# Kernel optimization log

Hardware: AMD Instinct MI355X
Metric: run time of the kernel (lower is better)

## Reference

```python
import jax, jax.numpy as jnp
import numpy as np

T, H, I, E, TOPK = 8192, 2048, 4096, 8, 2

def setup_inputs() -> dict:
    key = jax.random.key(0)
    k1, k2, k3, k4 = jax.random.split(key, 4)
    x = jax.random.normal(k1, (T, H), dtype=jnp.float32)
    gate_w = jax.random.normal(k2, (E, H), dtype=jnp.float32) * 0.02
    ws = jax.random.normal(k3, (E, 2 * I, H), dtype=jnp.float32) * 0.02
    w2s = jax.random.normal(k4, (E, H, I), dtype=jnp.float32) * 0.02
    return {"x": x, "gate_w": gate_w, "ws": ws, "w2s": w2s, "top_k": TOPK}

def reference(x, gate_w, ws, w2s, top_k):
    num_tokens = x.shape[0]
    num_experts = ws.shape[0]
    inter = w2s.shape[2]
    # --- router (fused_topk): softmax -> top-k -> renormalize ---
    logits = x @ gate_w.T                       # [T, E]
    probs = jax.nn.softmax(logits, axis=-1)
    topk_w, topk_ids = jax.lax.top_k(probs, top_k)   # [T, K]
    if top_k > 1:
        topk_w = topk_w / jnp.sum(topk_w, axis=-1, keepdims=True)
    # dense combine-weights [E, T]: sum of routing weights per (token, expert)
    tok = jnp.arange(num_tokens)
    cw = jnp.zeros((num_tokens, num_experts), dtype=x.dtype)
    cw = cw.at[tok[:, None], topk_ids].add(topk_w)
    cw = cw.T                                   # [E, T]
    # --- fused_experts: per-expert gated-SiLU MLP, weighted combine ---
    def body(acc, inp):
        e_ws, e_w2, e_cw = inp                  # [2I,H], [H,I], [T]
        gu = x @ e_ws.T                         # [T, 2I]
        g, u = gu[:, :inter], gu[:, inter:]
        h = jax.nn.silu(g) * u                  # SiluAndMul
        out = h @ e_w2.T                        # [T, H]
        return acc + e_cw[:, None] * out, None
    init = jnp.zeros_like(x)
    final, _ = jax.lax.scan(body, init, (ws, w2s, cw))
    return final
```

## Files before the change

### kernel.cpp

```cpp
#include <hip/hip_runtime.h>
#include <hip/hip_fp16.h>
#include <cstdint>
#include <cstddef>

#define TTOK 8192
#define HD   2048
#define ID   4096
#define NE   8
#define NPAIR (TTOK * 2)
#define PADROWS 18432
#define RBMAX 72

typedef _Float16 h8 __attribute__((ext_vector_type(8)));
typedef float    f4 __attribute__((ext_vector_type(4)));

#define VMWAIT(n) asm volatile("s_waitcnt vmcnt(" #n ")" ::: "memory")
#define MEMFENCE  asm volatile("" ::: "memory")
#define BAR()     __builtin_amdgcn_s_barrier()

__device__ __forceinline__ void async_cp16(const void* g, void* l) {
  __builtin_amdgcn_global_load_lds(
      (const __attribute__((address_space(1))) unsigned int*)g,
      (__attribute__((address_space(3))) unsigned int*)l, 16, 0, 0);
}

__device__ __forceinline__ f4 zero4() { f4 z = {0.f, 0.f, 0.f, 0.f}; return z; }

template <bool NT>
__global__ void cvt_kernel(const float* __restrict__ src, _Float16* __restrict__ dst, size_t n) {
  size_t stride = (size_t)gridDim.x * blockDim.x * 8;
  for (size_t i = ((size_t)blockIdx.x * blockDim.x + threadIdx.x) * 8; i < n; i += stride) {
    const float4* s = (const float4*)(src + i);
    float4 a = s[0], b = s[1];
    h8 o;
    o[0] = (_Float16)a.x; o[1] = (_Float16)a.y; o[2] = (_Float16)a.z; o[3] = (_Float16)a.w;
    o[4] = (_Float16)b.x; o[5] = (_Float16)b.y; o[6] = (_Float16)b.z; o[7] = (_Float16)b.w;
    if constexpr (NT) __builtin_nontemporal_store(o, (h8*)(dst + i));
    else *(h8*)(dst + i) = o;
  }
}

__global__ __launch_bounds__(256) void gate_kernel(
    const float* __restrict__ x, const float* __restrict__ gw,
    int* __restrict__ counts, int* __restrict__ tids, float* __restrict__ tw) {
  int lane = threadIdx.x & 63;
  int t = blockIdx.x * 4 + (threadIdx.x >> 6);
  const float* xr = x + (size_t)t * HD;
  float acc[NE];
#pragma unroll
  for (int e = 0; e < NE; e++) acc[e] = 0.f;
  for (int j = lane; j < HD; j += 64) {
    float xv = xr[j];
#pragma unroll
    for (int e = 0; e < NE; e++) acc[e] += xv * gw[e * HD + j];
  }
#pragma unroll
  for (int off = 32; off > 0; off >>= 1) {
#pragma unroll
    for (int e = 0; e < NE; e++) acc[e] += __shfl_xor(acc[e], off, 64);
  }
  if (lane == 0) {
    int e0 = 0; float v0 = acc[0];
#pragma unroll
    for (int e = 1; e < NE; e++) if (acc[e] > v0) { v0 = acc[e]; e0 = e; }
    int e1 = -1; float v1 = -1e30f;
#pragma unroll
    for (int e = 0; e < NE; e++) if (e != e0 && acc[e] > v1) { v1 = acc[e]; e1 = e; }
    float b = __expf(v1 - v0);
    float w0 = 1.f / (1.f + b);
    tids[2 * t] = e0; tids[2 * t + 1] = e1;
    tw[2 * t] = w0;   tw[2 * t + 1] = b * w0;
    atomicAdd(&counts[e0], 1); atomicAdd(&counts[e1], 1);
  }
}

__global__ void scan_kernel(const int* __restrict__ counts, int* __restrict__ offs,
                            int* __restrict__ cursor) {
  if (threadIdx.x == 0 && blockIdx.x == 0) {
    int off = 0;
    for (int e = 0; e < NE; e++) {
      offs[e] = off; cursor[e] = off;
      off += ((counts[e] + 255) >> 8) << 8;
    }
    offs[NE] = off;
  }
}

__global__ void scatter_kernel(const int* __restrict__ tids, const float* __restrict__ tw,
                               int* __restrict__ cursor, int* __restrict__ perm,
                               float* __restrict__ pw, int* __restrict__ pairpos) {
  int t = blockIdx.x * 256 + threadIdx.x;
#pragma unroll
  for (int k = 0; k < 2; k++) {
    int e = tids[2 * t + k];
    int pos = atomicAdd(&cursor[e], 1);
    perm[pos] = t; pw[pos] = tw[2 * t + k];
    pairpos[2 * t + k] = pos;
  }
}

__global__ void padfill_kernel(const int* __restrict__ counts, const int* __restrict__ offs,
                               int* __restrict__ perm) {
  int s = blockIdx.x * 256 + threadIdx.x;
#pragma unroll
  for (int e = 0; e < NE; e++) {
    if (s >= offs[e] + counts[e] && s < offs[e + 1]) perm[s] = -1;
  }
}

#define LA(BB, H) ((BB) * 65536 + (H) * 16384)
#define LB(BB, H) ((BB) * 65536 + 32768 + (H) * 16384)
#define RD(boff) (*(const h8*)(smem + (boff)))

#define LOAD_AF(BB, MH) do { \
  af[0][0] = RD(LA(BB,MH) + amoff + 0*2048 + sa0); \
  af[0][1] = RD(LA(BB,MH) + amoff + 0*2048 + sa1); \
  af[1][0] = RD(LA(BB,MH) + amoff + 1*2048 + sa0); \
  af[1][1] = RD(LA(BB,MH) + amoff + 1*2048 + sa1); \
  af[2][0] = RD(LA(BB,MH) + amoff + 2*2048 + sa0); \
  af[2][1] = RD(LA(BB,MH) + amoff + 2*2048 + sa1); \
  af[3][0] = RD(LA(BB,MH) + amoff + 3*2048 + sa0); \
  af[3][1] = RD(LA(BB,MH) + amoff + 3*2048 + sa1); } while (0)

#define LOAD_BF(BB, NH) do { \
  bf[0][0] = RD(LB(BB,NH) + bnoff + 0*2048 + sa0); \
  bf[0][1] = RD(LB(BB,NH) + bnoff + 0*2048 + sa1); \
  bf[1][0] = RD(LB(BB,NH) + bnoff + 1*2048 + sa0); \
  bf[1][1] = RD(LB(BB,NH) + bnoff + 1*2048 + sa1); } while (0)

#define MM(MH,NH,M,N) \
  acc[MH][NH][M][N] = __builtin_amdgcn_mfma_f32_16x16x32_f16(af[M][0], bf[N][0], acc[MH][NH][M][N], 0, 0, 0); \
  acc[MH][NH][M][N] = __builtin_amdgcn_mfma_f32_16x16x32_f16(af[M][1], bf[N][1], acc[MH][NH][M][N], 0, 0, 0);

#define MFMAQ(MH,NH) do { __builtin_amdgcn_s_setprio(1); \
  MM(MH,NH,0,0) MM(MH,NH,0,1) MM(MH,NH,1,0) MM(MH,NH,1,1) \
  MM(MH,NH,2,0) MM(MH,NH,2,1) MM(MH,NH,3,0) MM(MH,NH,3,1) \
  __builtin_amdgcn_s_setprio(0); } while (0)

#define STG(gp, ldsbyte, kt) do { \
  async_cp16(gp[0] + (size_t)(kt) * 64, smem + (ldsbyte) + (wid * 2 + 0) * 1024 + lane * 16); \
  async_cp16(gp[1] + (size_t)(kt) * 64, smem + (ldsbyte) + (wid * 2 + 1) * 1024 + lane * 16); } while (0)

#define ACC_ZERO() do { \
  _Pragma("unroll") for (int mh = 0; mh < 2; mh++) \
  _Pragma("unroll") for (int nh = 0; nh < 2; nh++) \
  _Pragma("unroll") for (int m = 0; m < 4; m++) \
  _Pragma("unroll") for (int n = 0; n < 2; n++) acc[mh][nh][m][n] = zero4(); } while (0)

#define KLOOP(NI) \
  STG(gA[0], LA(0,0), 0); STG(gA[1], LA(0,1), 0); \
  STG(gB[0], LB(0,0), 0); STG(gB[1], LB(0,1), 0); \
  STG(gA[0], LA(1,0), 1); STG(gB[1], LB(1,1), 1); \
  VMWAIT(4); \
  BAR(); \
  for (int i = 0; i < (NI); ++i) { \
    bool last = (i == (NI) - 1); \
    int kt1 = 2 * i + 1, kt2 = 2 * i + 2, kt3 = 2 * i + 3; \
     \
    MEMFENCE; LOAD_AF(0,0); LOAD_BF(0,0); \
    STG(gA[1], LA(1,1), kt1); STG(gB[0], LB(1,0), kt1); \
    BAR(); MEMFENCE; MFMAQ(0,0); BAR(); \
     \
    MEMFENCE; LOAD_BF(0,1); \
    BAR(); MEMFENCE; MFMAQ(0,1); BAR(); \
     \
    MEMFENCE; LOAD_AF(0,1); \
    if (!last) STG(gA[0], LA(0,0), kt2); \
    BAR(); MEMFENCE; MFMAQ(1,1); BAR(); \
     \
    MEMFENCE; LOAD_BF(0,0); \
    if (!last) { STG(gB[1], LB(0,1), kt2); VMWAIT(4); } else { VMWAIT(0); } \
    BAR(); MEMFENCE; MFMAQ(1,0); BAR(); \
     \
    MEMFENCE; LOAD_AF(1,0); LOAD_BF(1,0); \
    if (!last) { STG(gA[1], LA(0,1), kt2); STG(gB[0], LB(0,0), kt2); } \
    BAR(); MEMFENCE; MFMAQ(0,0); BAR(); \
     \
    MEMFENCE; LOAD_BF(1,1); \
    BAR(); MEMFENCE; MFMAQ(0,1); BAR(); \
     \
    MEMFENCE; LOAD_AF(1,1); \
    if (!last) STG(gA[0], LA(1,0), kt3); \
    BAR(); MEMFENCE; MFMAQ(1,1); BAR(); \
     \
    MEMFENCE; LOAD_BF(1,0); \
    if (!last) { STG(gB[1], LB(1,1), kt3); VMWAIT(4); } \
    BAR(); MEMFENCE; MFMAQ(1,0); BAR(); \
  }

__device__ __forceinline__ int expert_of(const int* offs, int row0) {
  int e = 0;
#pragma unroll
  for (int k = 1; k < NE; k++) if (offs[k] <= row0) e = k;
  return e;
}

__global__ __launch_bounds__(512, 2) void gemm1_kernel(
    const _Float16* __restrict__ xh, const _Float16* __restrict__ wsh,
    const int* __restrict__ offs, const int* __restrict__ perm,
    _Float16* __restrict__ hb) {
  int lin = blockIdx.x + gridDim.x * blockIdx.y;
  int oct = lin >> 8, x8 = lin & 7, bx = (lin >> 3) & 31;
  int gyy = oct * 8 + x8;
  int row0 = gyy << 8;
  if (row0 >= offs[NE]) return;
  int e = expert_of(offs, row0);
  int n0 = bx << 7;

  __shared__ char smem[131072];
  int tid = threadIdx.x, lane = tid & 63, wid = tid >> 6;
  int wm = wid >> 2, wn = wid & 3;
  int lr = lane & 15, ks = lane >> 4;
  int sa0 = lr * 128 + (((ks)     ^ (lr & 7)) << 4);
  int sa1 = lr * 128 + (((ks + 4) ^ (lr & 7)) << 4);
  int amoff = wm * 8192;
  int bnoff = wn * 4096;

  int srow = wid * 16 + (lane >> 3);
  int scol = ((lane & 7) ^ (lane >> 3)) * 8;
  const _Float16* gA[2][2]; const _Float16* gB[2][2];
#pragma unroll
  for (int h = 0; h < 2; h++)
#pragma unroll
    for (int j = 0; j < 2; j++) {
      int r = row0 + h * 128 + srow + j * 8;
      int pv = perm[r]; if (pv < 0) pv = 0;
      gA[h][j] = xh + (size_t)pv * HD + scol;
      gB[h][j] = wsh + ((size_t)e * 2 * ID + (size_t)h * ID + n0 + srow + j * 8) * HD + scol;
    }

  f4 acc[2][2][4][2];
  h8 af[4][2], bf[2][2];
  ACC_ZERO();

  KLOOP(16)

#pragma unroll
  for (int mh = 0; mh < 2; mh++)
#pragma unroll
    for (int m = 0; m < 4; m++)
#pragma unroll
      for (int n = 0; n < 2; n++)
#pragma unroll
        for (int r = 0; r < 4; r++) {
          float g = acc[mh][0][m][n][r], u = acc[mh][1][m][n][r];
          float hv = g / (1.f + __expf(-g)) * u;
          int row = row0 + mh * 128 + wm * 64 + m * 16 + ks * 4 + r;
          int col = n0 + wn * 32 + n * 16 + lr;
          __builtin_nontemporal_store((_Float16)hv, hb + (size_t)row * ID + col);
        }
}

__global__ __launch_bounds__(512, 2) void gemm2_kernel(
    const _Float16* __restrict__ hb, const _Float16* __restrict__ w2h,
    const int* __restrict__ offs, _Float16* __restrict__ hb2) {
  int lin = blockIdx.x + gridDim.x * blockIdx.y;
  int oct = lin >> 6, x8 = lin & 7, bx = (lin >> 3) & 7;
  int gyy = oct * 8 + x8;
  int row0 = gyy << 8;
  if (row0 >= offs[NE]) return;
  int e = expert_of(offs, row0);
  int n0 = bx << 8;
  int kh = blockIdx.z;
  size_t k0 = (size_t)kh * 2048;

  __shared__ char smem[131072];
  int tid = threadIdx.x, lane = tid & 63, wid = tid >> 6;
  int wm = wid >> 2, wn = wid & 3;
  int lr = lane & 15, ks = lane >> 4;
  int sa0 = lr * 128 + (((ks)     ^ (lr & 7)) << 4);
  int sa1 = lr * 128 + (((ks + 4) ^ (lr & 7)) << 4);
  int amoff = wm * 8192;
  int bnoff = wn * 4096;

  int srow = wid * 16 + (lane >> 3);
  int scol = ((lane & 7) ^ (lane >> 3)) * 8;
  const _Float16* gA[2][2]; const _Float16* gB[2][2];
#pragma unroll
  for (int h = 0; h < 2; h++)
#pragma unroll
    for (int j = 0; j < 2; j++) {
      gA[h][j] = hb + ((size_t)(row0 + h * 128 + srow + j * 8)) * ID + k0 + scol;
      gB[h][j] = w2h + ((size_t)e * HD + n0 + h * 128 + srow + j * 8) * ID + k0 + scol;
    }

  f4 acc[2][2][4][2];
  h8 af[4][2], bf[2][2];
  ACC_ZERO();

  KLOOP(16)

  _Float16* dst = hb2 + (size_t)kh * PADROWS * HD;
#pragma unroll
  for (int mh = 0; mh < 2; mh++)
#pragma unroll
    for (int nh = 0; nh < 2; nh++)
#pragma unroll
      for (int m = 0; m < 4; m++)
#pragma unroll
        for (int n = 0; n < 2; n++)
#pragma unroll
          for (int r = 0; r < 4; r++) {
            int row = row0 + mh * 128 + wm * 64 + m * 16 + ks * 4 + r;
            int col = n0 + nh * 128 + wn * 32 + n * 16 + lr;
            dst[(size_t)row * HD + col] = (_Float16)acc[mh][nh][m][n][r];
          }
}

__global__ __launch_bounds__(256) void combine_kernel(
    const _Float16* __restrict__ hb2, const int* __restrict__ pairpos,
    const float* __restrict__ pw, float* __restrict__ out) {
  int i = blockIdx.x * 256 + threadIdx.x;
  int t = i >> 8, g = (i & 255) * 8;
  int p0 = pairpos[2 * t], p1 = pairpos[2 * t + 1];
  float w0 = pw[p0], w1 = pw[p1];
  const _Float16* hb2b = hb2 + (size_t)PADROWS * HD;
  h8 a0 = *(const h8*)(hb2  + (size_t)p0 * HD + g);
  h8 a1 = *(const h8*)(hb2b + (size_t)p0 * HD + g);
  h8 b0 = *(const h8*)(hb2  + (size_t)p1 * HD + g);
  h8 b1 = *(const h8*)(hb2b + (size_t)p1 * HD + g);
  f4 o0, o1;
#pragma unroll
  for (int j = 0; j < 4; j++)
    o0[j] = w0 * ((float)a0[j] + (float)a1[j]) + w1 * ((float)b0[j] + (float)b1[j]);
#pragma unroll
  for (int j = 0; j < 4; j++)
    o1[j] = w0 * ((float)a0[j + 4] + (float)a1[j + 4]) + w1 * ((float)b0[j + 4] + (float)b1[j + 4]);
  __builtin_nontemporal_store(o0, (f4*)(out + (size_t)t * HD + g));
  __builtin_nontemporal_store(o1, (f4*)(out + (size_t)t * HD + g + 4));
}

extern "C" void kernel_launch(void* const* d_in, const int* in_sizes, int n_in,
                              void* d_out, int out_size, void* d_ws, size_t ws_size,
                              hipStream_t stream) {
  const float* x   = (const float*)d_in[0];
  const float* gw  = (const float*)d_in[1];
  const float* wsf = (const float*)d_in[2];
  const float* w2f = (const float*)d_in[3];

  int* counts   = (int*)d_ws;
  int* offs     = counts + 8;
  int* cursor   = offs + 16;
  int* tids     = cursor + 8;
  float* tw     = (float*)(tids + NPAIR);
  int* perm     = (int*)(tw + NPAIR);
  float* pw     = (float*)(perm + PADROWS);
  int* pairpos  = (int*)(pw + PADROWS);

  char* base = (char*)d_ws;
  size_t off_xh  = (size_t)512 * 1024;
  size_t off_hb  = off_xh + (size_t)TTOK * HD * 2;
  size_t off_big = off_hb + (size_t)PADROWS * ID * 2;
  size_t nws = (size_t)NE * 2 * ID * HD;
  size_t nw2 = (size_t)NE * HD * ID;
  size_t hb2_bytes = (size_t)2 * PADROWS * HD * 2;
  size_t big_bytes = nws * 2;
  size_t alt_bytes = nw2 * 2 + hb2_bytes;
  size_t need = off_big + (big_bytes > alt_bytes ? big_bytes : alt_bytes);
  if (ws_size < need) return;

  _Float16* xh  = (_Float16*)(base + off_xh);
  _Float16* hb  = (_Float16*)(base + off_hb);
  _Float16* wsh = (_Float16*)(base + off_big);
  _Float16* w2h = (_Float16*)(base + off_big);
  _Float16* hb2 = (_Float16*)(base + off_big + nw2 * 2);

  hipMemsetAsync(counts, 0, 64, stream);

  cvt_kernel<false><<<2048, 256, 0, stream>>>(x, xh, (size_t)TTOK * HD);
  cvt_kernel<true><<<4096, 256, 0, stream>>>(wsf, wsh, nws);
  gate_kernel<<<TTOK / 4, 256, 0, stream>>>(x, gw, counts, tids, tw);
  scan_kernel<<<1, 64, 0, stream>>>(counts, offs, cursor);
  scatter_kernel<<<TTOK / 256, 256, 0, stream>>>(tids, tw, cursor, perm, pw, pairpos);
  padfill_kernel<<<PADROWS / 256, 256, 0, stream>>>(counts, offs, perm);

  gemm1_kernel<<<dim3(ID / 128, RBMAX), 512, 0, stream>>>(
      xh, wsh, offs, perm, hb);

  cvt_kernel<false><<<4096, 256, 0, stream>>>(w2f, w2h, nw2);

  gemm2_kernel<<<dim3(HD / 256, RBMAX, 2), 512, 0, stream>>>(
      hb, w2h, offs, hb2);

  combine_kernel<<<(TTOK * HD / 8) / 256, 256, 0, stream>>>(
      hb2, pairpos, pw, (float*)d_out);
}
```

Measured before the change: 1.426 ms.

## Overlap w2 fp16 conversion with GEMM blocks and split gemm2 by K half

Removes the standalone w2 conversion kernel. The first K-half of w2 is now converted by extra blocks appended to the gemm1 grid, and the second half by extra blocks in the first gemm2 launch. gemm2 is split into two launches, one per K half, reading a compact 2048-wide w2 layout. The gemm1 grid-swizzle remapping is dropped, the B fragments get separate gate and up registers so one LDS reload per half-step is skipped, and workspace gains a dedicated w2h0 buffer. The trade-offs are higher register pressure, conversion blocks competing with GEMM tiles, and possibly worse L2 locality without the swizzle.

```diff
diff --git a/kernel.cpp b/kernel.cpp
--- a/kernel.cpp
+++ b/kernel.cpp
@@ -40,6 +40,22 @@
   }
 }
 
+__device__ __forceinline__ void cvt_w2_half(const float* __restrict__ w2f,
+                                            _Float16* __restrict__ dst,
+                                            int kh, int cb, int ncb) {
+  const size_t n = (size_t)NE * HD * 2048;
+  size_t stride = (size_t)ncb * 512 * 8;
+  for (size_t j = ((size_t)cb * 512 + threadIdx.x) * 8; j < n; j += stride) {
+    size_t row = j >> 11, ic = j & 2047;
+    const float4* s = (const float4*)(w2f + row * ID + (size_t)kh * 2048 + ic);
+    float4 a = s[0], b = s[1];
+    h8 o;
+    o[0] = (_Float16)a.x; o[1] = (_Float16)a.y; o[2] = (_Float16)a.z; o[3] = (_Float16)a.w;
+    o[4] = (_Float16)b.x; o[5] = (_Float16)b.y; o[6] = (_Float16)b.z; o[7] = (_Float16)b.w;
+    *(h8*)(dst + row * 2048 + ic) = o;
+  }
+}
+
 __global__ __launch_bounds__(256) void gate_kernel(
     const float* __restrict__ x, const float* __restrict__ gw,
     int* __restrict__ counts, int* __restrict__ tids, float* __restrict__ tw) {
@@ -122,19 +138,25 @@
   af[3][0] = RD(LA(BB,MH) + amoff + 3*2048 + sa0); \
   af[3][1] = RD(LA(BB,MH) + amoff + 3*2048 + sa1); } while (0)
 
-#define LOAD_BF(BB, NH) do { \
-  bf[0][0] = RD(LB(BB,NH) + bnoff + 0*2048 + sa0); \
-  bf[0][1] = RD(LB(BB,NH) + bnoff + 0*2048 + sa1); \
-  bf[1][0] = RD(LB(BB,NH) + bnoff + 1*2048 + sa0); \
-  bf[1][1] = RD(LB(BB,NH) + bnoff + 1*2048 + sa1); } while (0)
-
-#define MM(MH,NH,M,N) \
-  acc[MH][NH][M][N] = __builtin_amdgcn_mfma_f32_16x16x32_f16(af[M][0], bf[N][0], acc[MH][NH][M][N], 0, 0, 0); \
-  acc[MH][NH][M][N] = __builtin_amdgcn_mfma_f32_16x16x32_f16(af[M][1], bf[N][1], acc[MH][NH][M][N], 0, 0, 0);
-
-#define MFMAQ(MH,NH) do { __builtin_amdgcn_s_setprio(1); \
-  MM(MH,NH,0,0) MM(MH,NH,0,1) MM(MH,NH,1,0) MM(MH,NH,1,1) \
-  MM(MH,NH,2,0) MM(MH,NH,2,1) MM(MH,NH,3,0) MM(MH,NH,3,1) \
+#define LOAD_BFG(BB) do { \
+  bfg[0][0] = RD(LB(BB,0) + bnoff + 0*2048 + sa0); \
+  bfg[0][1] = RD(LB(BB,0) + bnoff + 0*2048 + sa1); \
+  bfg[1][0] = RD(LB(BB,0) + bnoff + 1*2048 + sa0); \
+  bfg[1][1] = RD(LB(BB,0) + bnoff + 1*2048 + sa1); } while (0)
+
+#define LOAD_BFU(BB) do { \
+  bfu[0][0] = RD(LB(BB,1) + bnoff + 0*2048 + sa0); \
+  bfu[0][1] = RD(LB(BB,1) + bnoff + 0*2048 + sa1); \
+  bfu[1][0] = RD(LB(BB,1) + bnoff + 1*2048 + sa0); \
+  bfu[1][1] = RD(LB(BB,1) + bnoff + 1*2048 + sa1); } while (0)
+
+#define MM(MH,NH,BF,M,N) \
+  acc[MH][NH][M][N] = __builtin_amdgcn_mfma_f32_16x16x32_f16(af[M][0], BF[N][0], acc[MH][NH][M][N], 0, 0, 0); \
+  acc[MH][NH][M][N] = __builtin_amdgcn_mfma_f32_16x16x32_f16(af[M][1], BF[N][1], acc[MH][NH][M][N], 0, 0, 0);
+
+#define MFMAQ(MH,NH,BF) do { __builtin_amdgcn_s_setprio(1); \
+  MM(MH,NH,BF,0,0) MM(MH,NH,BF,0,1) MM(MH,NH,BF,1,0) MM(MH,NH,BF,1,1) \
+  MM(MH,NH,BF,2,0) MM(MH,NH,BF,2,1) MM(MH,NH,BF,3,0) MM(MH,NH,BF,3,1) \
   __builtin_amdgcn_s_setprio(0); } while (0)
 
 #define STG(gp, ldsbyte, kt) do { \
@@ -157,35 +179,35 @@
     bool last = (i == (NI) - 1); \
     int kt1 = 2 * i + 1, kt2 = 2 * i + 2, kt3 = 2 * i + 3; \
      \
-    MEMFENCE; LOAD_AF(0,0); LOAD_BF(0,0); \
+    MEMFENCE; LOAD_AF(0,0); LOAD_BFG(0); \
     STG(gA[1], LA(1,1), kt1); STG(gB[0], LB(1,0), kt1); \
-    BAR(); MEMFENCE; MFMAQ(0,0); BAR(); \
-     \
-    MEMFENCE; LOAD_BF(0,1); \
-    BAR(); MEMFENCE; MFMAQ(0,1); BAR(); \
+    BAR(); MEMFENCE; MFMAQ(0,0,bfg); BAR(); \
+     \
+    MEMFENCE; LOAD_BFU(0); \
+    BAR(); MEMFENCE; MFMAQ(0,1,bfu); BAR(); \
      \
     MEMFENCE; LOAD_AF(0,1); \
     if (!last) STG(gA[0], LA(0,0), kt2); \
-    BAR(); MEMFENCE; MFMAQ(1,1); BAR(); \
-     \
-    MEMFENCE; LOAD_BF(0,0); \
+    BAR(); MEMFENCE; MFMAQ(1,1,bfu); BAR(); \
+     \
+    MEMFENCE; \
     if (!last) { STG(gB[1], LB(0,1), kt2); VMWAIT(4); } else { VMWAIT(0); } \
-    BAR(); MEMFENCE; MFMAQ(1,0); BAR(); \
-     \
-    MEMFENCE; LOAD_AF(1,0); LOAD_BF(1,0); \
+    BAR(); MEMFENCE; MFMAQ(1,0,bfg); BAR(); \
+     \
+    MEMFENCE; LOAD_AF(1,0); LOAD_BFG(1); \
     if (!last) { STG(gA[1], LA(0,1), kt2); STG(gB[0], LB(0,0), kt2); } \
-    BAR(); MEMFENCE; MFMAQ(0,0); BAR(); \
-     \
-    MEMFENCE; LOAD_BF(1,1); \
-    BAR(); MEMFENCE; MFMAQ(0,1); BAR(); \
+    BAR(); MEMFENCE; MFMAQ(0,0,bfg); BAR(); \
+     \
+    MEMFENCE; LOAD_BFU(1); \
+    BAR(); MEMFENCE; MFMAQ(0,1,bfu); BAR(); \
      \
     MEMFENCE; LOAD_AF(1,1); \
     if (!last) STG(gA[0], LA(1,0), kt3); \
-    BAR(); MEMFENCE; MFMAQ(1,1); BAR(); \
-     \
-    MEMFENCE; LOAD_BF(1,0); \
+    BAR(); MEMFENCE; MFMAQ(1,1,bfu); BAR(); \
+     \
+    MEMFENCE; \
     if (!last) { STG(gB[1], LB(1,1), kt3); VMWAIT(4); } \
-    BAR(); MEMFENCE; MFMAQ(1,0); BAR(); \
+    BAR(); MEMFENCE; MFMAQ(1,0,bfg); BAR(); \
   }
 
 __device__ __forceinline__ int expert_of(const int* offs, int row0) {
@@ -198,10 +220,13 @@
 __global__ __launch_bounds__(512, 2) void gemm1_kernel(
     const _Float16* __restrict__ xh, const _Float16* __restrict__ wsh,
     const int* __restrict__ offs, const int* __restrict__ perm,
-    _Float16* __restrict__ hb) {
-  int lin = blockIdx.x + gridDim.x * blockIdx.y;
-  int oct = lin >> 8, x8 = lin & 7, bx = (lin >> 3) & 31;
-  int gyy = oct * 8 + x8;
+    _Float16* __restrict__ hb,
+    const float* __restrict__ w2f, _Float16* __restrict__ w2h0) {
+  int bx = blockIdx.x, gyy = blockIdx.y;
+  if (gyy >= RBMAX) {
+    cvt_w2_half(w2f, w2h0, 0, (gyy - RBMAX) * 32 + bx, 256);
+    return;
+  }
   int row0 = gyy << 8;
   if (row0 >= offs[NE]) return;
   int e = expert_of(offs, row0);
@@ -230,7 +255,7 @@
     }
 
   f4 acc[2][2][4][2];
-  h8 af[4][2], bf[2][2];
+  h8 af[4][2], bfg[2][2], bfu[2][2];
   ACC_ZERO();
 
   KLOOP(16)
@@ -252,16 +277,18 @@
 }
 
 __global__ __launch_bounds__(512, 2) void gemm2_kernel(
-    const _Float16* __restrict__ hb, const _Float16* __restrict__ w2h,
-    const int* __restrict__ offs, _Float16* __restrict__ hb2) {
-  int lin = blockIdx.x + gridDim.x * blockIdx.y;
-  int oct = lin >> 6, x8 = lin & 7, bx = (lin >> 3) & 7;
-  int gyy = oct * 8 + x8;
+    const _Float16* __restrict__ hb, const _Float16* __restrict__ w2hk,
+    const int* __restrict__ offs, _Float16* __restrict__ hb2k, int kh,
+    const float* __restrict__ w2f, _Float16* __restrict__ w2h_other) {
+  int bx = blockIdx.x, gyy = blockIdx.y;
+  if (gyy >= RBMAX) {
+    cvt_w2_half(w2f, w2h_other, 1, (gyy - RBMAX) * 8 + bx, 64);
+    return;
+  }
   int row0 = gyy << 8;
   if (row0 >= offs[NE]) return;
   int e = expert_of(offs, row0);
   int n0 = bx << 8;
-  int kh = blockIdx.z;
   size_t k0 = (size_t)kh * 2048;
 
   __shared__ char smem[131072];
@@ -281,16 +308,15 @@
 #pragma unroll
     for (int j = 0; j < 2; j++) {
       gA[h][j] = hb + ((size_t)(row0 + h * 128 + srow + j * 8)) * ID + k0 + scol;
-      gB[h][j] = w2h + ((size_t)e * HD + n0 + h * 128 + srow + j * 8) * ID + k0 + scol;
+      gB[h][j] = w2hk + ((size_t)e * HD + n0 + h * 128 + srow + j * 8) * 2048 + scol;
     }
 
   f4 acc[2][2][4][2];
-  h8 af[4][2], bf[2][2];
+  h8 af[4][2], bfg[2][2], bfu[2][2];
   ACC_ZERO();
 
   KLOOP(16)
 
-  _Float16* dst = hb2 + (size_t)kh * PADROWS * HD;
 #pragma unroll
   for (int mh = 0; mh < 2; mh++)
 #pragma unroll
@@ -303,7 +329,7 @@
           for (int r = 0; r < 4; r++) {
             int row = row0 + mh * 128 + wm * 64 + m * 16 + ks * 4 + r;
             int col = n0 + nh * 128 + wn * 32 + n * 16 + lr;
-            dst[(size_t)row * HD + col] = (_Float16)acc[mh][nh][m][n][r];
+            hb2k[(size_t)row * HD + col] = (_Float16)acc[mh][nh][m][n][r];
           }
 }
 
@@ -348,39 +374,37 @@
   int* pairpos  = (int*)(pw + PADROWS);
 
   char* base = (char*)d_ws;
-  size_t off_xh  = (size_t)512 * 1024;
-  size_t off_hb  = off_xh + (size_t)TTOK * HD * 2;
-  size_t off_big = off_hb + (size_t)PADROWS * ID * 2;
-  size_t nws = (size_t)NE * 2 * ID * HD;
-  size_t nw2 = (size_t)NE * HD * ID;
-  size_t hb2_bytes = (size_t)2 * PADROWS * HD * 2;
-  size_t big_bytes = nws * 2;
-  size_t alt_bytes = nw2 * 2 + hb2_bytes;
-  size_t need = off_big + (big_bytes > alt_bytes ? big_bytes : alt_bytes);
+  size_t off_xh   = (size_t)512 * 1024;
+  size_t off_hb   = off_xh + (size_t)TTOK * HD * 2;
+  size_t off_w2h0 = off_hb + (size_t)PADROWS * ID * 2;
+  size_t off_big  = off_w2h0 + (size_t)NE * HD * 2048 * 2;
+  size_t need     = off_big + (size_t)NE * 2 * ID * HD * 2;
   if (ws_size < need) return;
 
-  _Float16* xh  = (_Float16*)(base + off_xh);
-  _Float16* hb  = (_Float16*)(base + off_hb);
-  _Float16* wsh = (_Float16*)(base + off_big);
-  _Float16* w2h = (_Float16*)(base + off_big);
-  _Float16* hb2 = (_Float16*)(base + off_big + nw2 * 2);
+  _Float16* xh   = (_Float16*)(base + off_xh);
+  _Float16* hb   = (_Float16*)(base + off_hb);
+  _Float16* w2h0 = (_Float16*)(base + off_w2h0);
+  _Float16* wsh  = (_Float16*)(base + off_big);
+  _Float16* w2h1 = (_Float16*)(base + off_big);
+  _Float16* hb2  = (_Float16*)(base + off_big + (size_t)NE * HD * 2048 * 2);
 
   hipMemsetAsync(counts, 0, 64, stream);
 
   cvt_kernel<false><<<2048, 256, 0, stream>>>(x, xh, (size_t)TTOK * HD);
-  cvt_kernel<true><<<4096, 256, 0, stream>>>(wsf, wsh, nws);
+  cvt_kernel<true><<<4096, 256, 0, stream>>>(wsf, wsh, (size_t)NE * 2 * ID * HD);
   gate_kernel<<<TTOK / 4, 256, 0, stream>>>(x, gw, counts, tids, tw);
   scan_kernel<<<1, 64, 0, stream>>>(counts, offs, cursor);
   scatter_kernel<<<TTOK / 256, 256, 0, stream>>>(tids, tw, cursor, perm, pw, pairpos);
   padfill_kernel<<<PADROWS / 256, 256, 0, stream>>>(counts, offs, perm);
 
-  gemm1_kernel<<<dim3(ID / 128, RBMAX), 512, 0, stream>>>(
-      xh, wsh, offs, perm, hb);
-
-  cvt_kernel<false><<<4096, 256, 0, stream>>>(w2f, w2h, nw2);
-
-  gemm2_kernel<<<dim3(HD / 256, RBMAX, 2), 512, 0, stream>>>(
-      hb, w2h, offs, hb2);
+  gemm1_kernel<<<dim3(ID / 128, RBMAX + 8), 512, 0, stream>>>(
+      xh, wsh, offs, perm, hb, w2f, w2h0);
+
+  gemm2_kernel<<<dim3(HD / 256, RBMAX + 8), 512, 0, stream>>>(
+      hb, w2h0, offs, hb2, 0, w2f, w2h1);
+
+  gemm2_kernel<<<dim3(HD / 256, RBMAX), 512, 0, stream>>>(
+      hb, w2h1, offs, hb2 + (size_t)PADROWS * HD, 1, w2f, (_Float16*)nullptr);
 
   combine_kernel<<<(TTOK * HD / 8) / 256, 256, 0, stream>>>(
       hb2, pairpos, pw, (float*)d_out);
```

New measurement: 1.439 ms. Within noise of the previous version (+0.9%).
